# Kernel tuning notes

Hardware: AMD Instinct MI355X
Metric: run time of the kernel (lower is better)

Reference implementation:

```python
import jax, jax.numpy as jnp
import numpy as np

T = 128          # target_size
START = 126      # tag_map['start_token']
STOP = 127       # tag_map['stop_token'] == 'end_token'
NEG = -10000.0


def setup_inputs() -> dict:
    key = jax.random.key(0)
    k1, k2, k3 = jax.random.split(key, 3)
    B, S = 256, 512
    feats = jax.random.normal(k1, (B, S, T), dtype=jnp.float32)
    transitions = jax.random.normal(k2, (T, T), dtype=jnp.float32)
    # constraints from __init__: nothing transitions into start, nothing leaves end
    transitions = transitions.at[START, :].set(NEG)
    transitions = transitions.at[:, STOP].set(NEG)
    targets = jax.random.randint(k3, (B, S), 0, 126, dtype=jnp.int32)
    return {"feats": feats, "transitions": transitions, "targets": targets}


def _crf_nll(feats, transitions, targets):
    B, S, _ = feats.shape
    # ---- forward algorithm (log partition) ----
    init = jnp.full((B, T), NEG, dtype=feats.dtype).at[:, START].set(0.0)

    def step(fv, f_t):  # fv [B,T], f_t [B,T]
        # new[b, tag] = logsumexp_prev(fv[b, prev] + trans[tag, prev]) + f_t[b, tag]
        new = jax.nn.logsumexp(fv[:, None, :] + transitions[None, :, :], axis=2) + f_t
        return new, None

    fv, _ = jax.lax.scan(step, init, jnp.swapaxes(feats, 0, 1))  # scan over S
    alpha = jax.nn.logsumexp(fv + transitions[STOP][None, :], axis=1)  # [B]

    # ---- gold path score ----
    start_col = jnp.full((B, 1), START, dtype=targets.dtype)
    tags_ext = jnp.concatenate([start_col, targets], axis=1)  # [B, S+1]
    trans_score = transitions[tags_ext[:, 1:], tags_ext[:, :-1]].sum(axis=1)  # [B]
    emit_score = jnp.take_along_axis(feats, targets[..., None].astype(jnp.int32), axis=2)[..., 0].sum(axis=1)
    gold = trans_score + emit_score + transitions[STOP, tags_ext[:, -1]]  # [B]

    # module returns gold_score - alpha
    return gold - alpha


def reference(feats, transitions, targets):
    return _crf_nll(feats, transitions, targets)
```

## Files before the change

kernel.cpp:

```cpp
#include <hip/hip_runtime.h>

#define TT 128
#define SS 512
#define NB 256
#define START_TAG 126
#define STOP_TAG 127
#define NEGV -10000.0f
#define LOG2E 1.4426950408889634f
#define LN2   0.6931471805599453f

typedef float v2 __attribute__((ext_vector_type(2)));

__device__ __forceinline__ float ex2(float x) { return __builtin_amdgcn_exp2f(x); }
__device__ __forceinline__ float lg2(float x) { return __builtin_amdgcn_logf(x); }
__device__ __forceinline__ float exn(float x) { return __builtin_amdgcn_exp2f(x * LOG2E); }

__device__ __forceinline__ float rlane(float v, int lane) {
    return __int_as_float(__builtin_amdgcn_readlane(__float_as_int(v), lane));
}
__device__ __forceinline__ float wave_max(float v) {
#pragma unroll
    for (int off = 32; off >= 1; off >>= 1) v = fmaxf(v, __shfl_xor(v, off));
    return v;
}
__device__ __forceinline__ float wave_sum(float v) {
#pragma unroll
    for (int off = 32; off >= 1; off >>= 1) v += __shfl_xor(v, off);
    return v;
}

__global__ __launch_bounds__(512, 2) void crf_fwd_kernel(
    const float* __restrict__ feats,
    const float* __restrict__ trans,
    const int*   __restrict__ targets,
    float*       __restrict__ out)
{
    const int t = threadIdx.x;
    const int b = blockIdx.x;
    const int w = t >> 6;
    const int l = t & 63;
    const int group = w >> 2;
    const int g = w & 3;
    const float gsel = group ? 0.f : 1.f;
    const float gnot = group ? 1.f : 0.f;

    __shared__ __align__(16) float pbuf[8][128];
    __shared__ v2 part[2][8][64];
    __shared__ float redz[8];
    __shared__ float galpha;

    v2 E2[32];
    if (group == 0) {
        const float* r0 = trans + l * TT + (g << 5);
        const float* r1 = trans + (l + 64) * TT + (g << 5);
#pragma unroll
        for (int k = 0; k < 32; k += 4) {
            float4 a0 = *reinterpret_cast<const float4*>(r0 + k);
            float4 a1 = *reinterpret_cast<const float4*>(r1 + k);
            E2[k + 0] = (v2){exn(a0.x), exn(a1.x)};
            E2[k + 1] = (v2){exn(a0.y), exn(a1.y)};
            E2[k + 2] = (v2){exn(a0.z), exn(a1.z)};
            E2[k + 3] = (v2){exn(a0.w), exn(a1.w)};
        }
    } else {
        const float* rc = trans + (g << 5) * TT + l;
#pragma unroll
        for (int k = 0; k < 32; ++k) {
            E2[k] = (v2){exn(rc[k * TT]), exn(rc[k * TT + 64])};
        }
    }

    const size_t bst = (size_t)b * (SS * TT);
    const float* fb = feats + bst + l;
    float* pwr = &pbuf[w][l];
    const float4* pq4 = reinterpret_cast<const float4*>(&pbuf[w][g << 5]);

#define FIDX(i) (group ? (510 - (i)) : (i))
    float fx0 = fb[(size_t)FIDX(0) * TT] * LOG2E, fy0 = fb[(size_t)FIDX(0) * TT + 64] * LOG2E;
    float fx1 = fb[(size_t)FIDX(1) * TT] * LOG2E, fy1 = fb[(size_t)FIDX(1) * TT + 64] * LOG2E;
    float fx2 = fb[(size_t)FIDX(2) * TT] * LOG2E, fy2 = fb[(size_t)FIDX(2) * TT + 64] * LOG2E;
    float fx3 = fb[(size_t)FIDX(3) * TT] * LOG2E, fy3 = fb[(size_t)FIDX(3) * TT + 64] * LOG2E;
    const int ii = group ? 511 : 0;
    float fInx = fb[(size_t)ii * TT] * LOG2E, fIny = fb[(size_t)ii * TT + 64] * LOG2E;
#undef FIDX

    float statex, statey;
    if (group == 0) {
        statex = NEGV;
        statey = (l == 62) ? 0.f : NEGV;
    } else {
        statex = trans[STOP_TAG * TT + l] * LOG2E;
        statey = trans[STOP_TAG * TT + l + 64] * LOG2E;
    }
    float argx = fmaf(fInx, gnot, statex);
    float argy = fmaf(fIny, gnot, statey);
    float M = group ? rlane(argx, 0) : 0.f;
    pwr[0]  = ex2(argx - M);
    pwr[64] = ex2(argy - M);

#define STEP(P)                                                             \
    {                                                                       \
        int sn = group ? (506 - s - (P)) : (s + 4 + (P));                   \
        float fnx = fb[(size_t)sn * TT] * LOG2E;                            \
        float fny = fb[(size_t)sn * TT + 64] * LOG2E;                       \
        v2 a0 = (v2){0.f, 0.f}, a1 = a0, a2 = a0, a3 = a0;                  \
        _Pragma("unroll")                                                   \
        for (int j = 0; j < 8; ++j) {                                       \
            float4 q = pq4[j];                                              \
            a0 = __builtin_elementwise_fma((v2){q.x, q.x}, E2[4*j+0], a0);  \
            a1 = __builtin_elementwise_fma((v2){q.y, q.y}, E2[4*j+1], a1);  \
            a2 = __builtin_elementwise_fma((v2){q.z, q.z}, E2[4*j+2], a2);  \
            a3 = __builtin_elementwise_fma((v2){q.w, q.w}, E2[4*j+3], a3);  \
        }                                                                   \
        v2 acc = (a0 + a1) + (a2 + a3);                                     \
        part[P][w][l] = acc;                                                \
        __syncthreads();                                                    \
        v2 c1 = part[P][w ^ 1][l];                                          \
        v2 c2 = part[P][w ^ 2][l];                                          \
        v2 c3 = part[P][w ^ 3][l];                                          \
        v2 tot = (acc + c1) + (c2 + c3);                                    \
        statex = fmaf(fx0, gsel, lg2(tot.x) + M);                           \
        statey = fmaf(fy0, gsel, lg2(tot.y) + M);                           \
        float agx = fmaf(fx0, gnot, statex);                                \
        float agy = fmaf(fy0, gnot, statey);                                \
        M = rlane(agx, 0);                                                  \
        pwr[0]  = ex2(agx - M);                                             \
        pwr[64] = ex2(agy - M);                                             \
        fx0 = fx1; fy0 = fy1; fx1 = fx2; fy1 = fy2;                         \
        fx2 = fx3; fy2 = fy3; fx3 = fnx; fy3 = fny;                         \
    }

    for (int s = 0; s < SS / 2; s += 2) {
        STEP(0)
        STEP(1)
    }
#undef STEP

    __syncthreads();
    if (w == 4) part[0][0][l] = (v2){statex, statey};

    {
        const int* tg = targets + b * SS;
        int cur  = tg[t];
        int prev = (t == 0) ? START_TAG : tg[t - 1];
        float gs = trans[cur * TT + prev] + feats[bst + (size_t)t * TT + cur];
        if (t == 0) gs += trans[STOP_TAG * TT + tg[SS - 1]];
        gs = wave_sum(gs);
        if (l == 0) redz[w] = gs;
    }
    __syncthreads();

    if (w == 0) {
        v2 bb = part[0][0][l];
        float vx = statex + bb.x;
        float vy = statey + bb.y;
        float m = wave_max(fmaxf(vx, vy));
        float e = ex2(vx - m) + ex2(vy - m);
        e = wave_sum(e);
        if (l == 0) galpha = (m + lg2(e)) * LN2;
    }
    __syncthreads();

    if (t == 0) {
        float gold = ((redz[0] + redz[1]) + (redz[2] + redz[3]))
                   + ((redz[4] + redz[5]) + (redz[6] + redz[7]));
        out[b] = gold - galpha;
    }
}

extern "C" void kernel_launch(void* const* d_in, const int* in_sizes, int n_in,
                              void* d_out, int out_size, void* d_ws, size_t ws_size,
                              hipStream_t stream) {
    const float* feats   = (const float*)d_in[0];
    const float* trans   = (const float*)d_in[1];
    const int*   targets = (const int*)d_in[2];
    float*       out     = (float*)d_out;
    crf_fwd_kernel<<<dim3(NB), dim3(512), 0, stream>>>(feats, trans, targets, out);
}
```

Baseline: 234.7 us.

## Run each CRF recursion direction in a single wave using readlane broadcasts

Replaces the four-wave-per-direction split, with its LDS partial sums and per-step block barrier, by a single wave per direction. Each wave keeps the full 128x128 exp-transition matrix in registers (256 floats per lane) and broadcasts the previous state with readlane. Two extra waves compute the gold path score in parallel. This removes the per-step __syncthreads and LDS traffic, but quadruples the serial FMA work per wave and risks very high register pressure or spilling.

```diff
diff --git a/kernel.cpp b/kernel.cpp
--- a/kernel.cpp
+++ b/kernel.cpp
@@ -29,7 +29,7 @@
     return v;
 }
 
-__global__ __launch_bounds__(512, 2) void crf_fwd_kernel(
+__global__ __launch_bounds__(256, 1) void crf_fwd_kernel(
     const float* __restrict__ feats,
     const float* __restrict__ trans,
     const int*   __restrict__ targets,
@@ -39,121 +39,127 @@
     const int b = blockIdx.x;
     const int w = t >> 6;
     const int l = t & 63;
-    const int group = w >> 2;
-    const int g = w & 3;
-    const float gsel = group ? 0.f : 1.f;
-    const float gnot = group ? 1.f : 0.f;
 
-    __shared__ __align__(16) float pbuf[8][128];
-    __shared__ v2 part[2][8][64];
-    __shared__ float redz[8];
+    __shared__ v2 bshare[64];
+    __shared__ float redz[4];
     __shared__ float galpha;
 
-    v2 E2[32];
-    if (group == 0) {
-        const float* r0 = trans + l * TT + (g << 5);
-        const float* r1 = trans + (l + 64) * TT + (g << 5);
+    const size_t bst = (size_t)b * (SS * TT);
+
+    v2 statev = (v2){0.f, 0.f};
+
+    if (w < 2) {
+        const int group = w;
+        const float gsel = group ? 0.f : 1.f;
+        const float gnot = group ? 1.f : 0.f;
+
+        v2 E2[128];
+        if (group == 0) {
+            const float* r0 = trans + l * TT;
+            const float* r1 = trans + (l + 64) * TT;
 #pragma unroll
-        for (int k = 0; k < 32; k += 4) {
-            float4 a0 = *reinterpret_cast<const float4*>(r0 + k);
-            float4 a1 = *reinterpret_cast<const float4*>(r1 + k);
-            E2[k + 0] = (v2){exn(a0.x), exn(a1.x)};
-            E2[k + 1] = (v2){exn(a0.y), exn(a1.y)};
-            E2[k + 2] = (v2){exn(a0.z), exn(a1.z)};
-            E2[k + 3] = (v2){exn(a0.w), exn(a1.w)};
+            for (int k = 0; k < 128; k += 4) {
+                float4 a0 = *reinterpret_cast<const float4*>(r0 + k);
+                float4 a1 = *reinterpret_cast<const float4*>(r1 + k);
+                E2[k + 0] = (v2){exn(a0.x), exn(a1.x)};
+                E2[k + 1] = (v2){exn(a0.y), exn(a1.y)};
+                E2[k + 2] = (v2){exn(a0.z), exn(a1.z)};
+                E2[k + 3] = (v2){exn(a0.w), exn(a1.w)};
+            }
+        } else {
+            const float* rc = trans + l;
+#pragma unroll
+            for (int k = 0; k < 128; ++k) {
+                E2[k] = (v2){exn(rc[k * TT]), exn(rc[k * TT + 64])};
+            }
         }
-    } else {
-        const float* rc = trans + (g << 5) * TT + l;
-#pragma unroll
-        for (int k = 0; k < 32; ++k) {
-            E2[k] = (v2){exn(rc[k * TT]), exn(rc[k * TT + 64])};
-        }
-    }
 
-    const size_t bst = (size_t)b * (SS * TT);
-    const float* fb = feats + bst + l;
-    float* pwr = &pbuf[w][l];
-    const float4* pq4 = reinterpret_cast<const float4*>(&pbuf[w][g << 5]);
+        const float* fb = feats + bst + l;
 
 #define FIDX(i) (group ? (510 - (i)) : (i))
-    float fx0 = fb[(size_t)FIDX(0) * TT] * LOG2E, fy0 = fb[(size_t)FIDX(0) * TT + 64] * LOG2E;
-    float fx1 = fb[(size_t)FIDX(1) * TT] * LOG2E, fy1 = fb[(size_t)FIDX(1) * TT + 64] * LOG2E;
-    float fx2 = fb[(size_t)FIDX(2) * TT] * LOG2E, fy2 = fb[(size_t)FIDX(2) * TT + 64] * LOG2E;
-    float fx3 = fb[(size_t)FIDX(3) * TT] * LOG2E, fy3 = fb[(size_t)FIDX(3) * TT + 64] * LOG2E;
-    const int ii = group ? 511 : 0;
-    float fInx = fb[(size_t)ii * TT] * LOG2E, fIny = fb[(size_t)ii * TT + 64] * LOG2E;
+        float fx0 = fb[(size_t)FIDX(0) * TT] * LOG2E, fy0 = fb[(size_t)FIDX(0) * TT + 64] * LOG2E;
+        float fx1 = fb[(size_t)FIDX(1) * TT] * LOG2E, fy1 = fb[(size_t)FIDX(1) * TT + 64] * LOG2E;
+        float fx2 = fb[(size_t)FIDX(2) * TT] * LOG2E, fy2 = fb[(size_t)FIDX(2) * TT + 64] * LOG2E;
+        float fx3 = fb[(size_t)FIDX(3) * TT] * LOG2E, fy3 = fb[(size_t)FIDX(3) * TT + 64] * LOG2E;
+        const int ii = group ? 511 : 0;
+        float fInx = fb[(size_t)ii * TT] * LOG2E, fIny = fb[(size_t)ii * TT + 64] * LOG2E;
 #undef FIDX
 
-    float statex, statey;
-    if (group == 0) {
-        statex = NEGV;
-        statey = (l == 62) ? 0.f : NEGV;
+        float statex, statey;
+        if (group == 0) {
+            statex = NEGV;
+            statey = (l == 62) ? 0.f : NEGV;
+        } else {
+            statex = trans[STOP_TAG * TT + l] * LOG2E;
+            statey = trans[STOP_TAG * TT + l + 64] * LOG2E;
+        }
+        float argx = fmaf(fInx, gnot, statex);
+        float argy = fmaf(fIny, gnot, statey);
+        float M = group ? rlane(argx, 0) : 0.f;
+        float px = ex2(argx - M);
+        float py = ex2(argy - M);
+
+        for (int s = 0; s < SS / 2; ++s) {
+            int sn = group ? (506 - s) : (s + 4);
+            float fnx = fb[(size_t)sn * TT] * LOG2E;
+            float fny = fb[(size_t)sn * TT + 64] * LOG2E;
+
+            v2 a0 = (v2){0.f, 0.f}, a1 = a0, a2 = a0, a3 = a0;
+#pragma unroll
+            for (int k = 0; k < 64; k += 4) {
+                float p0 = rlane(px, k + 0);
+                float p1 = rlane(px, k + 1);
+                float p2 = rlane(px, k + 2);
+                float p3 = rlane(px, k + 3);
+                a0 = __builtin_elementwise_fma((v2){p0, p0}, E2[k + 0], a0);
+                a1 = __builtin_elementwise_fma((v2){p1, p1}, E2[k + 1], a1);
+                a2 = __builtin_elementwise_fma((v2){p2, p2}, E2[k + 2], a2);
+                a3 = __builtin_elementwise_fma((v2){p3, p3}, E2[k + 3], a3);
+            }
+#pragma unroll
+            for (int k = 0; k < 64; k += 4) {
+                float p0 = rlane(py, k + 0);
+                float p1 = rlane(py, k + 1);
+                float p2 = rlane(py, k + 2);
+                float p3 = rlane(py, k + 3);
+                a0 = __builtin_elementwise_fma((v2){p0, p0}, E2[64 + k + 0], a0);
+                a1 = __builtin_elementwise_fma((v2){p1, p1}, E2[64 + k + 1], a1);
+                a2 = __builtin_elementwise_fma((v2){p2, p2}, E2[64 + k + 2], a2);
+                a3 = __builtin_elementwise_fma((v2){p3, p3}, E2[64 + k + 3], a3);
+            }
+            v2 tot = (a0 + a1) + (a2 + a3);
+
+            statex = fmaf(fx0, gsel, lg2(tot.x) + M);
+            statey = fmaf(fy0, gsel, lg2(tot.y) + M);
+            float agx = fmaf(fx0, gnot, statex);
+            float agy = fmaf(fy0, gnot, statey);
+            M = rlane(agx, 0);
+            px = ex2(agx - M);
+            py = ex2(agy - M);
+
+            fx0 = fx1; fy0 = fy1; fx1 = fx2; fy1 = fy2;
+            fx2 = fx3; fy2 = fy3; fx3 = fnx; fy3 = fny;
+        }
+        statev = (v2){statex, statey};
+        if (group == 1) bshare[l] = statev;
     } else {
-        statex = trans[STOP_TAG * TT + l] * LOG2E;
-        statey = trans[STOP_TAG * TT + l + 64] * LOG2E;
-    }
-    float argx = fmaf(fInx, gnot, statex);
-    float argy = fmaf(fIny, gnot, statey);
-    float M = group ? rlane(argx, 0) : 0.f;
-    pwr[0]  = ex2(argx - M);
-    pwr[64] = ex2(argy - M);
-
-#define STEP(P)                                                             \
-    {                                                                       \
-        int sn = group ? (506 - s - (P)) : (s + 4 + (P));                   \
-        float fnx = fb[(size_t)sn * TT] * LOG2E;                            \
-        float fny = fb[(size_t)sn * TT + 64] * LOG2E;                       \
-        v2 a0 = (v2){0.f, 0.f}, a1 = a0, a2 = a0, a3 = a0;                  \
-        _Pragma("unroll")                                                   \
-        for (int j = 0; j < 8; ++j) {                                       \
-            float4 q = pq4[j];                                              \
-            a0 = __builtin_elementwise_fma((v2){q.x, q.x}, E2[4*j+0], a0);  \
-            a1 = __builtin_elementwise_fma((v2){q.y, q.y}, E2[4*j+1], a1);  \
-            a2 = __builtin_elementwise_fma((v2){q.z, q.z}, E2[4*j+2], a2);  \
-            a3 = __builtin_elementwise_fma((v2){q.w, q.w}, E2[4*j+3], a3);  \
-        }                                                                   \
-        v2 acc = (a0 + a1) + (a2 + a3);                                     \
-        part[P][w][l] = acc;                                                \
-        __syncthreads();                                                    \
-        v2 c1 = part[P][w ^ 1][l];                                          \
-        v2 c2 = part[P][w ^ 2][l];                                          \
-        v2 c3 = part[P][w ^ 3][l];                                          \
-        v2 tot = (acc + c1) + (c2 + c3);                                    \
-        statex = fmaf(fx0, gsel, lg2(tot.x) + M);                           \
-        statey = fmaf(fy0, gsel, lg2(tot.y) + M);                           \
-        float agx = fmaf(fx0, gnot, statex);                                \
-        float agy = fmaf(fy0, gnot, statey);                                \
-        M = rlane(agx, 0);                                                  \
-        pwr[0]  = ex2(agx - M);                                             \
-        pwr[64] = ex2(agy - M);                                             \
-        fx0 = fx1; fy0 = fy1; fx1 = fx2; fy1 = fy2;                         \
-        fx2 = fx3; fy2 = fy3; fx3 = fnx; fy3 = fny;                         \
-    }
-
-    for (int s = 0; s < SS / 2; s += 2) {
-        STEP(0)
-        STEP(1)
-    }
-#undef STEP
-
-    __syncthreads();
-    if (w == 4) part[0][0][l] = (v2){statex, statey};
-
-    {
         const int* tg = targets + b * SS;
-        int cur  = tg[t];
-        int prev = (t == 0) ? START_TAG : tg[t - 1];
-        float gs = trans[cur * TT + prev] + feats[bst + (size_t)t * TT + cur];
-        if (t == 0) gs += trans[STOP_TAG * TT + tg[SS - 1]];
+        float gs = 0.f;
+        for (int i = t - 128; i < SS; i += 128) {
+            int cur  = tg[i];
+            int prev = (i == 0) ? START_TAG : tg[i - 1];
+            gs += trans[cur * TT + prev] + feats[bst + (size_t)i * TT + cur];
+        }
+        if (t == 128) gs += trans[STOP_TAG * TT + tg[SS - 1]];
         gs = wave_sum(gs);
         if (l == 0) redz[w] = gs;
     }
     __syncthreads();
 
     if (w == 0) {
-        v2 bb = part[0][0][l];
-        float vx = statex + bb.x;
-        float vy = statey + bb.y;
+        v2 bb = bshare[l];
+        float vx = statev.x + bb.x;
+        float vy = statev.y + bb.y;
         float m = wave_max(fmaxf(vx, vy));
         float e = ex2(vx - m) + ex2(vy - m);
         e = wave_sum(e);
@@ -161,11 +167,7 @@
     }
     __syncthreads();
 
-    if (t == 0) {
-        float gold = ((redz[0] + redz[1]) + (redz[2] + redz[3]))
-                   + ((redz[4] + redz[5]) + (redz[6] + redz[7]));
-        out[b] = gold - galpha;
-    }
+    if (t == 0) out[b] = (redz[2] + redz[3]) - galpha;
 }
 
 extern "C" void kernel_launch(void* const* d_in, const int* in_sizes, int n_in,
@@ -175,5 +177,5 @@
     const float* trans   = (const float*)d_in[1];
     const int*   targets = (const int*)d_in[2];
     float*       out     = (float*)d_out;
-    crf_fwd_kernel<<<dim3(NB), dim3(512), 0, stream>>>(feats, trans, targets, out);
+    crf_fwd_kernel<<<dim3(NB), dim3(256), 0, stream>>>(feats, trans, targets, out);
 }
```

New measurement: 372.0 us. +58.5%, slower.
